# Performance work log

Measured on AMD Instinct MI355X. Metric: run time of the kernel, lower is better.

Reference implementation:

```python
import jax, jax.numpy as jnp
import numpy as np

DIA = 2  # dilation of the 3x3 shift pattern


def setup_inputs() -> dict:
    key = jax.random.key(0)
    ks = jax.random.split(key, 6)
    B, C, H, W = 8, 3, 512, 512
    return {
        "x": jax.random.normal(ks[0], (B, C, H, W), dtype=jnp.float32),
        "y": jax.random.normal(ks[1], (B, C, 2 * H, 2 * W), dtype=jnp.float32),
        "w1": jax.random.normal(ks[2], (C,), dtype=jnp.float32) * 0.1,
        "b1": jax.random.normal(ks[3], (C,), dtype=jnp.float32) * 0.1,
        "w2": jax.random.normal(ks[4], (C,), dtype=jnp.float32) * 0.1,
        "b2": jax.random.normal(ks[5], (C,), dtype=jnp.float32) * 0.1,
    }


def _per_channel(x, w, b):
    # grouped 1x1 conv with groups == channels == per-channel scale + bias
    return x * w[None, :, None, None] + b[None, :, None, None]


def reference(x, y, w1, b1, w2, b2):
    D = DIA
    h, w = x.shape[2], x.shape[3]
    # conv1 is applied twice to the same input -> x_o == x_r
    x_o = jax.nn.relu(_per_channel(x, w1, b1))
    x_r = x_o
    # 9-way shifted zero-padded sum == dilated 3x3 box-sum
    pad = jnp.pad(x_o, ((0, 0), (0, 0), (D, D), (D, D)))
    out_n = jnp.zeros_like(x_o)
    for i in range(3):
        for j in range(3):
            out_n = out_n + pad[:, :, i * D:i * D + h, j * D:j * D + w]
    gate = jax.nn.sigmoid(_per_channel(out_n, w2, b2))
    out = gate * x_r
    # F.interpolate default mode='nearest': src = floor(dst * in / out)
    H2, W2 = y.shape[2], y.shape[3]
    ih = (jnp.arange(H2) * h) // H2
    iw = (jnp.arange(W2) * w) // W2
    up = out[:, :, ih, :][:, :, :, iw]
    return y + up
```

## Files before the change

kernel.cpp:

```cpp
#include <hip/hip_runtime.h>


#define DIA 2

__global__ __launch_bounds__(256) void fused_kernel(
    const float* __restrict__ x, const float* __restrict__ y,
    const float* __restrict__ w1v, const float* __restrict__ b1v,
    const float* __restrict__ w2v, const float* __restrict__ b2v,
    float* __restrict__ out)
{
    constexpr int C = 3, H = 512, W = 512, W2 = 1024;
    constexpr int NBLK = 12288, CHUNK = NBLK / 8;

    int g = blockIdx.x;
    int l = (g & 7) * CHUNK + (g >> 3);

    int idx = l * 256 + threadIdx.x;
    int wp = idx & (W / 2 - 1);
    int h  = __builtin_amdgcn_readfirstlane((idx >> 8) & (H - 1));
    int bc = __builtin_amdgcn_readfirstlane(idx >> 17);
    int c  = bc % C;
    int w0 = wp * 2;

    const float s_w1 = w1v[c], s_b1 = b1v[c];
    const float s_w2 = w2v[c], s_b2 = b2v[c];

    const float* __restrict__ xrow = x + ((size_t)bc * H + (size_t)h) * W;

    const bool ok0 = (h >= DIA), ok2 = (h < H - DIA);
    const bool lok = (w0 > 0), rok = (w0 + 2 < W);
    const float m0 = ok0 ? 1.f : 0.f;
    const float m2 = ok2 ? 1.f : 0.f;
    const float mL = lok ? 1.f : 0.f;
    const float mR = rok ? 1.f : 0.f;

    const float* r1 = xrow;
    const float* r0 = ok0 ? (xrow - DIA * W) : xrow;
    const float* r2 = ok2 ? (xrow + DIA * W) : xrow;
    const int wl = lok ? (w0 - 2) : w0;
    const int wr = rok ? (w0 + 2) : w0;

    float2 L0 = *(const float2*)(r0 + wl);
    float2 M0 = *(const float2*)(r0 + w0);
    float2 R0 = *(const float2*)(r0 + wr);
    float2 L1 = *(const float2*)(r1 + wl);
    float2 M1 = *(const float2*)(r1 + w0);
    float2 R1 = *(const float2*)(r1 + wr);
    float2 L2 = *(const float2*)(r2 + wl);
    float2 M2 = *(const float2*)(r2 + w0);
    float2 R2 = *(const float2*)(r2 + wr);

    size_t obase = (((size_t)bc * (2 * H) + (size_t)(2 * h)) * W2) + (size_t)(2 * w0);
    float4 ya = *(const float4*)(y + obase);
    float4 yb = *(const float4*)(y + obase + W2);

    auto act = [&](float v) { return fmaxf(fmaf(v, s_w1, s_b1), 0.f); };

    float xo0 = act(M1.x);
    float xo1 = act(M1.y);

    float sum0 = mL * act(L1.x) + xo0 + mR * act(R1.x);
    float sum1 = mL * act(L1.y) + xo1 + mR * act(R1.y);
    sum0 += m0 * (mL * act(L0.x) + act(M0.x) + mR * act(R0.x));
    sum1 += m0 * (mL * act(L0.y) + act(M0.y) + mR * act(R0.y));
    sum0 += m2 * (mL * act(L2.x) + act(M2.x) + mR * act(R2.x));
    sum1 += m2 * (mL * act(L2.y) + act(M2.y) + mR * act(R2.y));

    float z0 = fmaf(sum0, s_w2, s_b2);
    float z1 = fmaf(sum1, s_w2, s_b2);
    float o0 = xo0 / (1.f + __expf(-z0));
    float o1 = xo1 / (1.f + __expf(-z1));

    *(float4*)(out + obase)      = make_float4(ya.x + o0, ya.y + o0, ya.z + o1, ya.w + o1);
    *(float4*)(out + obase + W2) = make_float4(yb.x + o0, yb.y + o0, yb.z + o1, yb.w + o1);
}

extern "C" void kernel_launch(void* const* d_in, const int* in_sizes, int n_in,
                              void* d_out, int out_size, void* d_ws, size_t ws_size,
                              hipStream_t stream) {
    const float* x  = (const float*)d_in[0];
    const float* y  = (const float*)d_in[1];
    const float* w1 = (const float*)d_in[2];
    const float* b1 = (const float*)d_in[3];
    const float* w2 = (const float*)d_in[4];
    const float* b2 = (const float*)d_in[5];
    float* out = (float*)d_out;

    constexpr int B = 8, C = 3, H = 512, W = 512;
    int total_threads = B * C * H * (W / 2);
    int block = 256;
    int grid  = total_threads / block;
    fused_kernel<<<grid, block, 0, stream>>>(x, y, w1, b1, w2, b2, out);
}
```

Before: 205.9 us.

## Process eight rows per block with double-buffered async y staging into LDS

Each block now loops over eight consecutive image rows instead of handling one. The y tile for the next row is prefetched into shared memory with global_load_lds while the current row is computed, so y loads overlap the stencil work. This cuts the grid to 1536 blocks and adds a barrier every row. The kernel remains memory-bound and the smaller grid may lower latency hiding, and x rows are still reloaded from global memory or cache without reuse across rows.

```diff
diff --git a/kernel.cpp b/kernel.cpp
--- a/kernel.cpp
+++ b/kernel.cpp
@@ -2,6 +2,9 @@
 
 
 #define DIA 2
+
+typedef __attribute__((address_space(3))) void lds_void;
+typedef const __attribute__((address_space(1))) void gmem_void;
 
 __global__ __launch_bounds__(256) void fused_kernel(
     const float* __restrict__ x, const float* __restrict__ y,
@@ -10,69 +13,95 @@
     float* __restrict__ out)
 {
     constexpr int C = 3, H = 512, W = 512, W2 = 1024;
-    constexpr int NBLK = 12288, CHUNK = NBLK / 8;
+    constexpr int ROWS = 8;
+    constexpr int BPI  = H / ROWS;
+    constexpr int NBLK = 24 * BPI;
+    constexpr int CHUNK = NBLK / 8;
+
+    __shared__ float ys[2][2 * W2];
 
     int g = blockIdx.x;
     int l = (g & 7) * CHUNK + (g >> 3);
 
-    int idx = l * 256 + threadIdx.x;
-    int wp = idx & (W / 2 - 1);
-    int h  = __builtin_amdgcn_readfirstlane((idx >> 8) & (H - 1));
-    int bc = __builtin_amdgcn_readfirstlane(idx >> 17);
-    int c  = bc % C;
-    int w0 = wp * 2;
+    int bc  = l / BPI;
+    int h0  = (l % BPI) * ROWS;
+    int c   = bc % C;
+    int tid = (int)threadIdx.x;
+    int w0  = tid * 2;
+    int lane = tid & 63;
+    int wv  = __builtin_amdgcn_readfirstlane(tid >> 6);
 
     const float s_w1 = w1v[c], s_b1 = b1v[c];
     const float s_w2 = w2v[c], s_b2 = b2v[c];
 
-    const float* __restrict__ xrow = x + ((size_t)bc * H + (size_t)h) * W;
+    const float* __restrict__ ximg = x + (size_t)bc * H * W;
+    const size_t ybase = (size_t)bc * (2 * H) * W2;
 
-    const bool ok0 = (h >= DIA), ok2 = (h < H - DIA);
     const bool lok = (w0 > 0), rok = (w0 + 2 < W);
-    const float m0 = ok0 ? 1.f : 0.f;
-    const float m2 = ok2 ? 1.f : 0.f;
     const float mL = lok ? 1.f : 0.f;
     const float mR = rok ? 1.f : 0.f;
-
-    const float* r1 = xrow;
-    const float* r0 = ok0 ? (xrow - DIA * W) : xrow;
-    const float* r2 = ok2 ? (xrow + DIA * W) : xrow;
     const int wl = lok ? (w0 - 2) : w0;
     const int wr = rok ? (w0 + 2) : w0;
 
-    float2 L0 = *(const float2*)(r0 + wl);
-    float2 M0 = *(const float2*)(r0 + w0);
-    float2 R0 = *(const float2*)(r0 + wr);
-    float2 L1 = *(const float2*)(r1 + wl);
-    float2 M1 = *(const float2*)(r1 + w0);
-    float2 R1 = *(const float2*)(r1 + wr);
-    float2 L2 = *(const float2*)(r2 + wl);
-    float2 M2 = *(const float2*)(r2 + w0);
-    float2 R2 = *(const float2*)(r2 + wr);
-
-    size_t obase = (((size_t)bc * (2 * H) + (size_t)(2 * h)) * W2) + (size_t)(2 * w0);
-    float4 ya = *(const float4*)(y + obase);
-    float4 yb = *(const float4*)(y + obase + W2);
+    auto stage = [&](int k, int buf) {
+        size_t yr = ybase + (size_t)(2 * (h0 + k)) * W2;
+        const float* gpa = y + yr +      wv * 256 + lane * 4;
+        const float* gpb = y + yr + W2 + wv * 256 + lane * 4;
+        __builtin_amdgcn_global_load_lds((gmem_void*)gpa,
+                                         (lds_void*)(&ys[buf][wv * 256]), 16, 0, 0);
+        __builtin_amdgcn_global_load_lds((gmem_void*)gpb,
+                                         (lds_void*)(&ys[buf][W2 + wv * 256]), 16, 0, 0);
+    };
 
     auto act = [&](float v) { return fmaxf(fmaf(v, s_w1, s_b1), 0.f); };
 
-    float xo0 = act(M1.x);
-    float xo1 = act(M1.y);
+    stage(0, 0);
 
-    float sum0 = mL * act(L1.x) + xo0 + mR * act(R1.x);
-    float sum1 = mL * act(L1.y) + xo1 + mR * act(R1.y);
-    sum0 += m0 * (mL * act(L0.x) + act(M0.x) + mR * act(R0.x));
-    sum1 += m0 * (mL * act(L0.y) + act(M0.y) + mR * act(R0.y));
-    sum0 += m2 * (mL * act(L2.x) + act(M2.x) + mR * act(R2.x));
-    sum1 += m2 * (mL * act(L2.y) + act(M2.y) + mR * act(R2.y));
+    for (int k = 0; k < ROWS; ++k) {
+        __syncthreads();
 
-    float z0 = fmaf(sum0, s_w2, s_b2);
-    float z1 = fmaf(sum1, s_w2, s_b2);
-    float o0 = xo0 / (1.f + __expf(-z0));
-    float o1 = xo1 / (1.f + __expf(-z1));
+        const int h = h0 + k;
+        const float* xrow = ximg + (size_t)h * W;
+        const bool ok0 = (h >= DIA), ok2 = (h < H - DIA);
+        const float m0 = ok0 ? 1.f : 0.f;
+        const float m2 = ok2 ? 1.f : 0.f;
+        const float* r0 = ok0 ? (xrow - DIA * W) : xrow;
+        const float* r2 = ok2 ? (xrow + DIA * W) : xrow;
 
-    *(float4*)(out + obase)      = make_float4(ya.x + o0, ya.y + o0, ya.z + o1, ya.w + o1);
-    *(float4*)(out + obase + W2) = make_float4(yb.x + o0, yb.y + o0, yb.z + o1, yb.w + o1);
+        float2 L0 = *(const float2*)(r0 + wl);
+        float2 M0 = *(const float2*)(r0 + w0);
+        float2 R0 = *(const float2*)(r0 + wr);
+        float2 L1 = *(const float2*)(xrow + wl);
+        float2 M1 = *(const float2*)(xrow + w0);
+        float2 R1 = *(const float2*)(xrow + wr);
+        float2 L2 = *(const float2*)(r2 + wl);
+        float2 M2 = *(const float2*)(r2 + w0);
+        float2 R2 = *(const float2*)(r2 + wr);
+
+        if (k + 1 < ROWS) stage(k + 1, (k + 1) & 1);
+
+        float4 ya = *(const float4*)&ys[k & 1][2 * w0];
+        float4 yb = *(const float4*)&ys[k & 1][W2 + 2 * w0];
+
+        float xo0 = act(M1.x);
+        float xo1 = act(M1.y);
+
+        float sum0 = mL * act(L1.x) + xo0 + mR * act(R1.x);
+        float sum1 = mL * act(L1.y) + xo1 + mR * act(R1.y);
+        sum0 += m0 * (mL * act(L0.x) + act(M0.x) + mR * act(R0.x));
+        sum1 += m0 * (mL * act(L0.y) + act(M0.y) + mR * act(R0.y));
+        sum0 += m2 * (mL * act(L2.x) + act(M2.x) + mR * act(R2.x));
+        sum1 += m2 * (mL * act(L2.y) + act(M2.y) + mR * act(R2.y));
+
+        float z0 = fmaf(sum0, s_w2, s_b2);
+        float z1 = fmaf(sum1, s_w2, s_b2);
+        float o0 = xo0 / (1.f + __expf(-z0));
+        float o1 = xo1 / (1.f + __expf(-z1));
+
+        size_t obase = ybase + (size_t)(2 * h) * W2 + (size_t)(2 * w0);
+        *(float4*)(out + obase)      = make_float4(ya.x + o0, ya.y + o0, ya.z + o1, ya.w + o1);
+        *(float4*)(out + obase + W2) = make_float4(yb.x + o0, yb.y + o0, yb.z + o1, yb.w + o1);
+    }
 }
 
 extern "C" void kernel_launch(void* const* d_in, const int* in_sizes, int n_in,
@@ -86,9 +115,6 @@
     const float* b2 = (const float*)d_in[5];
     float* out = (float*)d_out;
 
-    constexpr int B = 8, C = 3, H = 512, W = 512;
-    int total_threads = B * C * H * (W / 2);
-    int block = 256;
-    int grid  = total_threads / block;
+    int grid = 1536, block = 256;
     fused_kernel<<<grid, block, 0, stream>>>(x, y, w1, b1, w2, b2, out);
 }
```

Result: slower. 219.6 us (+6.7%).
